# Kernel tuning notes

Hardware: AMD Instinct MI355X
Metric: run time of the kernel (lower is better)

## Reference

```python
import jax, jax.numpy as jnp
import numpy as np

LR = 0.01
BETA1 = 0.9
BETA2 = 0.999
EPS = 1e-08
V = 1_000_000   # num_embeddings
D = 64          # embedding_dim
N = 524_288     # number of gradient rows


def setup_inputs() -> dict:
    key = jax.random.key(0)
    k1, k2, k3, k4, k5 = jax.random.split(key, 5)
    idx = jax.random.randint(k1, (N,), 0, V)
    grad = jax.random.normal(k2, (N, D), jnp.float32)
    emb = jax.random.normal(k3, (V, D), jnp.float32)
    state_step = jnp.zeros((V,), jnp.float32)
    state_mem = jax.random.normal(k4, (V, D), jnp.float32)
    state_power = jax.random.uniform(k5, (V, D), jnp.float32)  # second moment must be >= 0
    return {"idx": idx, "grad": grad, "emb": emb,
            "state_step": state_step, "state_mem": state_mem, "state_power": state_power}


def reference(idx, grad, emb, state_step, state_mem, state_power):
    """Fused sparse-Adam update. Equivalent to torch unique+index_add dedup,
    gather of per-row Adam state, elementwise Adam math, scatter-back.
    Implemented jit-compatibly with fixed-size segment sums over the full table;
    untouched rows are masked so they are returned unchanged (same semantics
    as the scatter-only torch version)."""
    v = emb.shape[0]
    # dedup: per-row count and summed gradient (== unique + index_add)
    cnt = jax.ops.segment_sum(jnp.ones(idx.shape, jnp.float32), idx, num_segments=v)   # [V]
    gsum = jax.ops.segment_sum(grad, idx, num_segments=v)                               # [V, D]
    touched = cnt > 0
    gv = gsum / jnp.where(touched, cnt, 1.0)[:, None]  # mean gradient per unique index

    step_new = jnp.where(touched, state_step + 1.0, state_step)
    mem_new = jnp.where(touched[:, None], BETA1 * state_mem + (1.0 - BETA1) * gv, state_mem)
    pow_new = jnp.where(touched[:, None], BETA2 * state_power + (1.0 - BETA2) * gv * gv, state_power)

    # bias correction (guard denominators for untouched rows with step==0)
    d1 = jnp.where(touched, 1.0 - BETA1 ** step_new, 1.0)
    d2 = jnp.where(touched, 1.0 - BETA2 ** step_new, 1.0)
    mem_corr = mem_new / d1[:, None]
    pow_corr = pow_new / d2[:, None]

    upd = LR * mem_corr / (jnp.sqrt(pow_corr) + EPS)
    emb_new = jnp.where(touched[:, None], emb - upd, emb)
    return emb_new, step_new, mem_new, pow_new
```

## Files before the change

### kernel.cpp

```cpp
#include <hip/hip_runtime.h>

#define LR    0.01f
#define B1    0.9f
#define B2    0.999f
#define EPSL  1e-8f

#define SCAN_CHUNK   1024
#define SCAN_THREADS 256

#define LOG2_B1 (-0.15200309344504997f)
#define LOG2_B2 (-0.0014434251880582487f)

__global__ void zero_cnt_kernel(int* __restrict__ cnt, int V) {
    int t = blockIdx.x * blockDim.x + threadIdx.x;
    int stride = gridDim.x * blockDim.x;
    for (int i = t; i < V; i += stride) cnt[i] = 0;
}

__global__ void count_kernel(const int* __restrict__ idx,
                             int* __restrict__ cnt,
                             int* __restrict__ rowpos, int N) {
    int i = blockIdx.x * blockDim.x + threadIdx.x;
    if (i >= N) return;
    int v = idx[i];
    rowpos[i] = atomicAdd(&cnt[v], 1);
}

__global__ void block_sum_kernel(const int* __restrict__ cnt,
                                 int* __restrict__ bsum, int V) {
    __shared__ int sh[SCAN_THREADS];
    int b = blockIdx.x, t = threadIdx.x;
    int base = b * SCAN_CHUNK + t * 4;
    int s = 0;
    #pragma unroll
    for (int k = 0; k < 4; ++k) {
        int i = base + k;
        if (i < V) s += cnt[i];
    }
    sh[t] = s;
    __syncthreads();
    for (int d = 128; d > 0; d >>= 1) {
        if (t < d) sh[t] += sh[t + d];
        __syncthreads();
    }
    if (t == 0) bsum[b] = sh[0];
}

__global__ void scan_bsum_kernel(const int* __restrict__ bsum,
                                 int* __restrict__ bpre, int nB) {
    __shared__ int sh[1024];
    int t = threadIdx.x;
    int own = (t < nB) ? bsum[t] : 0;
    sh[t] = own;
    __syncthreads();
    for (int d = 1; d < 1024; d <<= 1) {
        int add = (t >= d) ? sh[t - d] : 0;
        __syncthreads();
        sh[t] += add;
        __syncthreads();
    }
    if (t < nB) bpre[t] = sh[t] - own;
}

__global__ void scan_apply_kernel(const int* __restrict__ cnt,
                                  const int* __restrict__ bpre,
                                  int* __restrict__ off, int V) {
    __shared__ int sh[SCAN_THREADS];
    int b = blockIdx.x, t = threadIdx.x;
    int base = b * SCAN_CHUNK + t * 4;
    int c[4];
    int s = 0;
    #pragma unroll
    for (int k = 0; k < 4; ++k) {
        int i = base + k;
        c[k] = (i < V) ? cnt[i] : 0;
        s += c[k];
    }
    int own = s;
    sh[t] = s;
    __syncthreads();
    for (int d = 1; d < 256; d <<= 1) {
        int add = (t >= d) ? sh[t - d] : 0;
        __syncthreads();
        sh[t] += add;
        __syncthreads();
    }
    int pre = bpre[b] + (sh[t] - own);
    #pragma unroll
    for (int k = 0; k < 4; ++k) {
        int i = base + k;
        if (i < V) off[i] = pre;
        pre += c[k];
    }
}

__global__ void fill_kernel(const int* __restrict__ idx,
                            const int* __restrict__ rowpos,
                            const int* __restrict__ off,
                            int* __restrict__ rowids, int N) {
    int i = blockIdx.x * blockDim.x + threadIdx.x;
    if (i >= N) return;
    int v = idx[i];
    rowids[off[v] + rowpos[i]] = i;
}

__global__ void adam_kernel(const float4* __restrict__ emb4,
                            const float*  __restrict__ step_in,
                            const float4* __restrict__ mem4,
                            const float4* __restrict__ pow4,
                            const float4* __restrict__ grad4,
                            const int*    __restrict__ cnt,
                            const int*    __restrict__ off,
                            const int*    __restrict__ rowids,
                            float* __restrict__ out,
                            int V) {
    int t = blockIdx.x * blockDim.x + threadIdx.x;
    int v = t >> 4;
    int q = t & 15;
    if (v >= V) return;

    float4* emb_out  = (float4*)out;
    float*  step_out = out + (long)V * 64;
    float4* mem_out  = (float4*)(out + (long)V * 64 + V);
    float4* pow_out  = mem_out + (long)V * 16;

    int c = cnt[v];
    int o = off[v];
    bool touched = (c > 0);

    float4 gs = make_float4(0.f, 0.f, 0.f, 0.f);
    for (int j = 0; j < c; ++j) {
        int r = rowids[o + j];
        float4 g = grad4[(long)r * 16 + q];
        gs.x += g.x; gs.y += g.y; gs.z += g.z; gs.w += g.w;
    }

    float4 e = emb4[t];
    float4 m = mem4[t];
    float4 p = pow4[t];
    float s_old = step_in[v];
    float s_new = touched ? s_old + 1.f : s_old;

    float inv_c = touched ? 1.f / (float)c : 0.f;
    float d1 = touched ? 1.f - exp2f(s_new * LOG2_B1) : 1.f;
    float d2 = touched ? 1.f - exp2f(s_new * LOG2_B2) : 1.f;
    float inv_d1 = 1.f / d1;
    float inv_d2 = 1.f / d2;

    float4 m_new, p_new, e_new;
    {
        float gv, mn, pn, upd;
        gv = gs.x * inv_c;
        mn = touched ? B1 * m.x + (1.f - B1) * gv : m.x;
        pn = touched ? B2 * p.x + (1.f - B2) * gv * gv : p.x;
        upd = LR * (mn * inv_d1) / (sqrtf(pn * inv_d2) + EPSL);
        m_new.x = mn; p_new.x = pn; e_new.x = touched ? e.x - upd : e.x;

        gv = gs.y * inv_c;
        mn = touched ? B1 * m.y + (1.f - B1) * gv : m.y;
        pn = touched ? B2 * p.y + (1.f - B2) * gv * gv : p.y;
        upd = LR * (mn * inv_d1) / (sqrtf(pn * inv_d2) + EPSL);
        m_new.y = mn; p_new.y = pn; e_new.y = touched ? e.y - upd : e.y;

        gv = gs.z * inv_c;
        mn = touched ? B1 * m.z + (1.f - B1) * gv : m.z;
        pn = touched ? B2 * p.z + (1.f - B2) * gv * gv : p.z;
        upd = LR * (mn * inv_d1) / (sqrtf(pn * inv_d2) + EPSL);
        m_new.z = mn; p_new.z = pn; e_new.z = touched ? e.z - upd : e.z;

        gv = gs.w * inv_c;
        mn = touched ? B1 * m.w + (1.f - B1) * gv : m.w;
        pn = touched ? B2 * p.w + (1.f - B2) * gv * gv : p.w;
        upd = LR * (mn * inv_d1) / (sqrtf(pn * inv_d2) + EPSL);
        m_new.w = mn; p_new.w = pn; e_new.w = touched ? e.w - upd : e.w;
    }

    emb_out[t] = e_new;
    mem_out[t] = m_new;
    pow_out[t] = p_new;
    if (q == 0) step_out[v] = s_new;
}

extern "C" void kernel_launch(void* const* d_in, const int* in_sizes, int n_in,
                              void* d_out, int out_size, void* d_ws, size_t ws_size,
                              hipStream_t stream) {
    const int*   idx  = (const int*)  d_in[0];
    const float* grad = (const float*)d_in[1];
    const float* emb  = (const float*)d_in[2];
    const float* step = (const float*)d_in[3];
    const float* mem  = (const float*)d_in[4];
    const float* pw   = (const float*)d_in[5];

    const int N = in_sizes[0];
    const int V = in_sizes[3];

    float* out = (float*)d_out;

    int* cnt    = (int*)d_ws;
    int* off    = cnt + V;
    int* rowpos = off + V;
    int* rowids = rowpos + N;
    int* bsum   = rowids + N;
    int* bpre   = bsum + 1024;

    const int nB = (V + SCAN_CHUNK - 1) / SCAN_CHUNK;

    zero_cnt_kernel<<<1024, 256, 0, stream>>>(cnt, V);
    count_kernel<<<(N + 255) / 256, 256, 0, stream>>>(idx, cnt, rowpos, N);
    block_sum_kernel<<<nB, SCAN_THREADS, 0, stream>>>(cnt, bsum, V);
    scan_bsum_kernel<<<1, 1024, 0, stream>>>(bsum, bpre, nB);
    scan_apply_kernel<<<nB, SCAN_THREADS, 0, stream>>>(cnt, bpre, off, V);
    fill_kernel<<<(N + 255) / 256, 256, 0, stream>>>(idx, rowpos, off, rowids, N);
    {
        long total = (long)V * 16;
        int threads = 256;
        int blocks = (int)((total + threads - 1) / threads);
        adam_kernel<<<blocks, threads, 0, stream>>>((const float4*)emb, step,
                                                    (const float4*)mem, (const float4*)pw,
                                                    (const float4*)grad,
                                                    cnt, off, rowids, out, V);
    }
}
```

Before: 363.4 us.

## Replace three-pass scan with atomic bucket allocation and use nontemporal loads/stores

The three-kernel exclusive scan that computed per-row offsets is replaced by one kernel that does a block-local scan and reserves a contiguous range with a single atomicAdd on a global cursor. Bucket offsets stay disjoint but are no longer in row order, which is fine because only the per-row ranges are used. The Adam kernel now uses nontemporal loads and stores for the streamed emb/mem/pow/grad data to reduce cache pollution. This saves two launches and a pass over cnt, at the cost of one contended atomic per block.

New measurement: 369.8 us. No clear change (+1.8%).

```diff
diff --git a/kernel.cpp b/kernel.cpp
--- a/kernel.cpp
+++ b/kernel.cpp
@@ -5,16 +5,15 @@
 #define B2    0.999f
 #define EPSL  1e-8f
 
-#define SCAN_CHUNK   1024
-#define SCAN_THREADS 256
-
 #define LOG2_B1 (-0.15200309344504997f)
 #define LOG2_B2 (-0.0014434251880582487f)
 
-__global__ void zero_cnt_kernel(int* __restrict__ cnt, int V) {
+typedef float f4 __attribute__((ext_vector_type(4)));
+
+__global__ void zero_cnt_kernel(int* __restrict__ cnt, int n) {
     int t = blockIdx.x * blockDim.x + threadIdx.x;
     int stride = gridDim.x * blockDim.x;
-    for (int i = t; i < V; i += stride) cnt[i] = 0;
+    for (int i = t; i < n; i += stride) cnt[i] = 0;
 }
 
 __global__ void count_kernel(const int* __restrict__ idx,
@@ -26,72 +25,26 @@
     rowpos[i] = atomicAdd(&cnt[v], 1);
 }
 
-__global__ void block_sum_kernel(const int* __restrict__ cnt,
-                                 int* __restrict__ bsum, int V) {
-    __shared__ int sh[SCAN_THREADS];
-    int b = blockIdx.x, t = threadIdx.x;
-    int base = b * SCAN_CHUNK + t * 4;
-    int s = 0;
+__global__ void alloc_kernel(const int* __restrict__ cnt,
+                             int* __restrict__ off,
+                             int* __restrict__ cursor, int V) {
+    __shared__ int sh[256];
+    __shared__ int sh_base;
+    int t = threadIdx.x;
+    int i = blockIdx.x * 256 + t;
+    int c = (i < V) ? cnt[i] : 0;
+    sh[t] = c;
+    __syncthreads();
     #pragma unroll
-    for (int k = 0; k < 4; ++k) {
-        int i = base + k;
-        if (i < V) s += cnt[i];
-    }
-    sh[t] = s;
-    __syncthreads();
-    for (int d = 128; d > 0; d >>= 1) {
-        if (t < d) sh[t] += sh[t + d];
-        __syncthreads();
-    }
-    if (t == 0) bsum[b] = sh[0];
-}
-
-__global__ void scan_bsum_kernel(const int* __restrict__ bsum,
-                                 int* __restrict__ bpre, int nB) {
-    __shared__ int sh[1024];
-    int t = threadIdx.x;
-    int own = (t < nB) ? bsum[t] : 0;
-    sh[t] = own;
-    __syncthreads();
-    for (int d = 1; d < 1024; d <<= 1) {
-        int add = (t >= d) ? sh[t - d] : 0;
-        __syncthreads();
-        sh[t] += add;
-        __syncthreads();
-    }
-    if (t < nB) bpre[t] = sh[t] - own;
-}
-
-__global__ void scan_apply_kernel(const int* __restrict__ cnt,
-                                  const int* __restrict__ bpre,
-                                  int* __restrict__ off, int V) {
-    __shared__ int sh[SCAN_THREADS];
-    int b = blockIdx.x, t = threadIdx.x;
-    int base = b * SCAN_CHUNK + t * 4;
-    int c[4];
-    int s = 0;
-    #pragma unroll
-    for (int k = 0; k < 4; ++k) {
-        int i = base + k;
-        c[k] = (i < V) ? cnt[i] : 0;
-        s += c[k];
-    }
-    int own = s;
-    sh[t] = s;
-    __syncthreads();
     for (int d = 1; d < 256; d <<= 1) {
         int add = (t >= d) ? sh[t - d] : 0;
         __syncthreads();
         sh[t] += add;
         __syncthreads();
     }
-    int pre = bpre[b] + (sh[t] - own);
-    #pragma unroll
-    for (int k = 0; k < 4; ++k) {
-        int i = base + k;
-        if (i < V) off[i] = pre;
-        pre += c[k];
-    }
+    if (t == 255) sh_base = atomicAdd(cursor, sh[255]);
+    __syncthreads();
+    if (i < V) off[i] = sh_base + sh[t] - c;
 }
 
 __global__ void fill_kernel(const int* __restrict__ idx,
@@ -104,14 +57,14 @@
     rowids[off[v] + rowpos[i]] = i;
 }
 
-__global__ void adam_kernel(const float4* __restrict__ emb4,
-                            const float*  __restrict__ step_in,
-                            const float4* __restrict__ mem4,
-                            const float4* __restrict__ pow4,
-                            const float4* __restrict__ grad4,
-                            const int*    __restrict__ cnt,
-                            const int*    __restrict__ off,
-                            const int*    __restrict__ rowids,
+__global__ void adam_kernel(const f4* __restrict__ emb4,
+                            const float* __restrict__ step_in,
+                            const f4* __restrict__ mem4,
+                            const f4* __restrict__ pow4,
+                            const f4* __restrict__ grad4,
+                            const int* __restrict__ cnt,
+                            const int* __restrict__ off,
+                            const int* __restrict__ rowids,
                             float* __restrict__ out,
                             int V) {
     int t = blockIdx.x * blockDim.x + threadIdx.x;
@@ -119,25 +72,25 @@
     int q = t & 15;
     if (v >= V) return;
 
-    float4* emb_out  = (float4*)out;
-    float*  step_out = out + (long)V * 64;
-    float4* mem_out  = (float4*)(out + (long)V * 64 + V);
-    float4* pow_out  = mem_out + (long)V * 16;
+    f4*    emb_out  = (f4*)out;
+    float* step_out = out + (long)V * 64;
+    f4*    mem_out  = (f4*)(out + (long)V * 64 + V);
+    f4*    pow_out  = mem_out + (long)V * 16;
 
     int c = cnt[v];
     int o = off[v];
     bool touched = (c > 0);
 
-    float4 gs = make_float4(0.f, 0.f, 0.f, 0.f);
+    f4 gs = {0.f, 0.f, 0.f, 0.f};
     for (int j = 0; j < c; ++j) {
         int r = rowids[o + j];
-        float4 g = grad4[(long)r * 16 + q];
-        gs.x += g.x; gs.y += g.y; gs.z += g.z; gs.w += g.w;
+        f4 g = __builtin_nontemporal_load(&grad4[(long)r * 16 + q]);
+        gs += g;
     }
 
-    float4 e = emb4[t];
-    float4 m = mem4[t];
-    float4 p = pow4[t];
+    f4 e = __builtin_nontemporal_load(&emb4[t]);
+    f4 m = __builtin_nontemporal_load(&mem4[t]);
+    f4 p = __builtin_nontemporal_load(&pow4[t]);
     float s_old = step_in[v];
     float s_new = touched ? s_old + 1.f : s_old;
 
@@ -147,37 +100,21 @@
     float inv_d1 = 1.f / d1;
     float inv_d2 = 1.f / d2;
 
-    float4 m_new, p_new, e_new;
-    {
-        float gv, mn, pn, upd;
-        gv = gs.x * inv_c;
-        mn = touched ? B1 * m.x + (1.f - B1) * gv : m.x;
-        pn = touched ? B2 * p.x + (1.f - B2) * gv * gv : p.x;
-        upd = LR * (mn * inv_d1) / (sqrtf(pn * inv_d2) + EPSL);
-        m_new.x = mn; p_new.x = pn; e_new.x = touched ? e.x - upd : e.x;
-
-        gv = gs.y * inv_c;
-        mn = touched ? B1 * m.y + (1.f - B1) * gv : m.y;
-        pn = touched ? B2 * p.y + (1.f - B2) * gv * gv : p.y;
-        upd = LR * (mn * inv_d1) / (sqrtf(pn * inv_d2) + EPSL);
-        m_new.y = mn; p_new.y = pn; e_new.y = touched ? e.y - upd : e.y;
-
-        gv = gs.z * inv_c;
-        mn = touched ? B1 * m.z + (1.f - B1) * gv : m.z;
-        pn = touched ? B2 * p.z + (1.f - B2) * gv * gv : p.z;
-        upd = LR * (mn * inv_d1) / (sqrtf(pn * inv_d2) + EPSL);
-        m_new.z = mn; p_new.z = pn; e_new.z = touched ? e.z - upd : e.z;
-
-        gv = gs.w * inv_c;
-        mn = touched ? B1 * m.w + (1.f - B1) * gv : m.w;
-        pn = touched ? B2 * p.w + (1.f - B2) * gv * gv : p.w;
-        upd = LR * (mn * inv_d1) / (sqrtf(pn * inv_d2) + EPSL);
-        m_new.w = mn; p_new.w = pn; e_new.w = touched ? e.w - upd : e.w;
+    f4 m_new, p_new, e_new;
+    #pragma unroll
+    for (int k = 0; k < 4; ++k) {
+        float gv = gs[k] * inv_c;
+        float mn = touched ? B1 * m[k] + (1.f - B1) * gv : m[k];
+        float pn = touched ? B2 * p[k] + (1.f - B2) * gv * gv : p[k];
+        float upd = LR * (mn * inv_d1) / (sqrtf(pn * inv_d2) + EPSL);
+        m_new[k] = mn;
+        p_new[k] = pn;
+        e_new[k] = touched ? e[k] - upd : e[k];
     }
 
-    emb_out[t] = e_new;
-    mem_out[t] = m_new;
-    pow_out[t] = p_new;
+    __builtin_nontemporal_store(e_new, &emb_out[t]);
+    __builtin_nontemporal_store(m_new, &mem_out[t]);
+    __builtin_nontemporal_store(p_new, &pow_out[t]);
     if (q == 0) step_out[v] = s_new;
 }
 
@@ -197,27 +134,22 @@
     float* out = (float*)d_out;
 
     int* cnt    = (int*)d_ws;
-    int* off    = cnt + V;
+    int* cursor = cnt + V;
+    int* off    = cursor + 1;
     int* rowpos = off + V;
     int* rowids = rowpos + N;
-    int* bsum   = rowids + N;
-    int* bpre   = bsum + 1024;
 
-    const int nB = (V + SCAN_CHUNK - 1) / SCAN_CHUNK;
-
-    zero_cnt_kernel<<<1024, 256, 0, stream>>>(cnt, V);
+    zero_cnt_kernel<<<1024, 256, 0, stream>>>(cnt, V + 1);
     count_kernel<<<(N + 255) / 256, 256, 0, stream>>>(idx, cnt, rowpos, N);
-    block_sum_kernel<<<nB, SCAN_THREADS, 0, stream>>>(cnt, bsum, V);
-    scan_bsum_kernel<<<1, 1024, 0, stream>>>(bsum, bpre, nB);
-    scan_apply_kernel<<<nB, SCAN_THREADS, 0, stream>>>(cnt, bpre, off, V);
+    alloc_kernel<<<(V + 255) / 256, 256, 0, stream>>>(cnt, off, cursor, V);
     fill_kernel<<<(N + 255) / 256, 256, 0, stream>>>(idx, rowpos, off, rowids, N);
     {
         long total = (long)V * 16;
         int threads = 256;
         int blocks = (int)((total + threads - 1) / threads);
-        adam_kernel<<<blocks, threads, 0, stream>>>((const float4*)emb, step,
-                                                    (const float4*)mem, (const float4*)pw,
-                                                    (const float4*)grad,
+        adam_kernel<<<blocks, threads, 0, stream>>>((const f4*)emb, step,
+                                                    (const f4*)mem, (const f4*)pw,
+                                                    (const f4*)grad,
                                                     cnt, off, rowids, out, V);
     }
 }
```
